# Kernel optimization log

Measured on AMD Instinct MI355X. Metric: run time of the kernel, lower is better.

Reference implementation:

```python
import jax, jax.numpy as jnp
import numpy as np

B, N_PER, E_PER = 100, 1000, 12000  # graphs, nodes/graph, edges/graph
N, E = B * N_PER, B * E_PER
K = int(np.ceil(0.8 * N_PER))  # TopKPooling ratio=0.8 -> 800 kept nodes/graph


def setup_inputs() -> dict:
    key = jax.random.key(0)
    ks = jax.random.split(key, 16)
    g = jnp.repeat(jnp.arange(B, dtype=jnp.int64), E_PER)
    src = g * N_PER + jax.random.randint(ks[0], (E,), 0, N_PER)
    dst = g * N_PER + jax.random.randint(ks[1], (E,), 0, N_PER)
    edge_index = jnp.stack([src, dst]).astype(jnp.int64)
    edge_attr = jax.random.uniform(ks[2], (E,), dtype=jnp.float32) + 0.1  # positive edge weights
    x = jax.random.normal(ks[3], (N, 3), dtype=jnp.float32)
    batch = jnp.repeat(jnp.arange(B, dtype=jnp.int64), N_PER)
    s = 0.1
    return {
        'x': x, 'edge_index': edge_index, 'edge_attr': edge_attr, 'batch': batch,
        'conv1_w': jax.random.normal(ks[4], (3, 64), dtype=jnp.float32) * s,
        'conv1_b': jnp.zeros((64,), dtype=jnp.float32),
        'conv2_w': jax.random.normal(ks[5], (64, 64), dtype=jnp.float32) * s,
        'conv2_b': jnp.zeros((64,), dtype=jnp.float32),
        'pool_w': jax.random.normal(ks[6], (64,), dtype=jnp.float32) * s,
        'lin1_w': jax.random.normal(ks[7], (64, 64), dtype=jnp.float32) * s,
        'lin1_b': jnp.zeros((64,), dtype=jnp.float32),
        'lin2_w': jax.random.normal(ks[8], (64, 32), dtype=jnp.float32) * s,
        'lin2_b': jnp.zeros((32,), dtype=jnp.float32),
        'lin3_w': jax.random.normal(ks[9], (32, 1), dtype=jnp.float32) * s,
        'lin3_b': jnp.zeros((1,), dtype=jnp.float32),
    }


def gcn_conv(x, row, col, ew, W, b):
    # PyG GCNConv with edge_weight and implicit self-loops (weight 1):
    # deg[i] = sum_{e: col=i} ew[e] + 1;  norm_e = d^{-1/2}[row]*ew*d^{-1/2}[col]
    h = x @ W  # [N, out]
    deg = jax.ops.segment_sum(ew, col, num_segments=N) + 1.0
    dinv = jax.lax.rsqrt(deg)
    msg = (dinv[row] * ew * dinv[col])[:, None] * h[row]  # [E, out]
    out = jax.ops.segment_sum(msg, col, num_segments=N)
    out = out + (dinv * dinv)[:, None] * h  # self-loop term
    return out + b


def reference(x, edge_index, edge_attr, batch, conv1_w, conv1_b, conv2_w, conv2_b,
              pool_w, lin1_w, lin1_b, lin2_w, lin2_b, lin3_w, lin3_b):
    row, col = edge_index[0], edge_index[1]
    h = jax.nn.relu(gcn_conv(x, row, col, edge_attr, conv1_w, conv1_b))
    x1 = h.reshape(B, N_PER, 64).mean(axis=1)  # global_mean_pool (equal-size graphs)
    h = jax.nn.relu(gcn_conv(h, row, col, edge_attr, conv2_w, conv2_b))
    # TopKPooling: score = tanh(x.w / ||w||), keep top-K per graph, gate by score
    score = jnp.tanh(h @ pool_w / jnp.linalg.norm(pool_w))  # [N]
    score_bn = score.reshape(B, N_PER)
    vals, idx = jax.lax.top_k(score_bn, K)  # [B, K]
    h_bn = h.reshape(B, N_PER, 64)
    h_sel = jnp.take_along_axis(h_bn, idx[..., None], axis=1) * vals[..., None]
    x2 = h_sel.mean(axis=1)  # global_mean_pool on pooled graph
    z = x1 + x2
    z = jax.nn.relu(z @ lin1_w + lin1_b)
    z = jax.nn.relu(z @ lin2_w + lin2_b)  # dropout is identity in eval mode
    out = jax.nn.sigmoid(z @ lin3_w + lin3_b)[:, 0]
    return out
```

## Files before the change

kernel.cpp:

```cpp
#include <hip/hip_runtime.h>

#define B_G   100
#define N_PER 1000
#define E_PER 12000
#define NTOT  (B_G * N_PER)
#define ETOT  (B_G * E_PER)
#define KSEL  800
#define EPT   12
#define NH    500
#define HCAP  8192

typedef __attribute__((ext_vector_type(8))) short short8;
typedef __attribute__((ext_vector_type(4))) float float4_;

__device__ __forceinline__ unsigned short f2bf(float f) {
    unsigned u = __float_as_uint(f);
    u += 0x7fffu + ((u >> 16) & 1u);
    return (unsigned short)(u >> 16);
}
__device__ __forceinline__ float upk(unsigned q) {
    return __uint_as_float(q & 0xFFFF0000u);
}
__device__ __forceinline__ float dec_raw(unsigned byte7f) {
    return __uint_as_float(byte7f << 20);
}
__device__ __forceinline__ unsigned enc_fp8(float z) {
    unsigned u = __float_as_uint(z * 0x1p-120f);
    u += 0x7FFFFu + ((u >> 20) & 1u);
    return u >> 20;
}

__global__ __launch_bounds__(1024) void k1_build(
    const int* __restrict__ ei, const float* __restrict__ ew,
    unsigned* __restrict__ csr_g, int* __restrict__ ends_g,
    float* __restrict__ dl_g) {
    __shared__ unsigned csr[E_PER];
    __shared__ int ends[1024];
    __shared__ int posc[1024];
    __shared__ int wpart[16];
    int b = blockIdx.x, tid = threadIdx.x;
    int wid = tid >> 6, lane = tid & 63;
    int gbase = b * N_PER, ebase = b * E_PER;

    int esrc[EPT], edst[EPT]; float eww[EPT];
    int ne = (tid < (E_PER - (EPT - 1) * 1024)) ? EPT : EPT - 1;
#pragma unroll
    for (int i = 0; i < EPT; i++) {
        if (i < ne) {
            int e = tid + i * 1024;
            esrc[i] = ei[ebase + e] - gbase;
            edst[i] = ei[ETOT + ebase + e] - gbase;
            eww[i]  = ew[ebase + e];
        }
    }
    ends[tid] = 0;
    __syncthreads();
#pragma unroll
    for (int i = 0; i < EPT; i++)
        if (i < ne) atomicAdd(&ends[edst[i]], 1);
    __syncthreads();
    int v = ends[tid], sc = v;
#pragma unroll
    for (int m = 1; m < 64; m <<= 1) {
        int t = __shfl_up(sc, m);
        if (lane >= m) sc += t;
    }
    if (lane == 63) wpart[wid] = sc;
    __syncthreads();
    if (tid < 16) {
        int s2 = wpart[tid];
#pragma unroll
        for (int m = 1; m < 16; m <<= 1) {
            int t = __shfl_up(s2, m);
            if (tid >= m) s2 += t;
        }
        wpart[tid] = s2;
    }
    __syncthreads();
    int incl = sc + (wid > 0 ? wpart[wid - 1] : 0);
    ends[tid] = incl;
    posc[tid] = incl - v;
    __syncthreads();
#pragma unroll
    for (int i = 0; i < EPT; i++)
        if (i < ne) {
            int p = atomicAdd(&posc[edst[i]], 1);
            csr[p] = ((unsigned)f2bf(eww[i]) << 16) | (unsigned)esrc[i];
        }
    __syncthreads();
    if (tid < N_PER) {
        int s = tid ? ends[tid - 1] : 0, e = ends[tid];
        float s0 = 0.f, s1 = 0.f;
        int k = s;
        for (; k + 2 <= e; k += 2) { s0 += upk(csr[k]); s1 += upk(csr[k + 1]); }
        if (k < e) s0 += upk(csr[k]);
        dl_g[gbase + tid] = rsqrtf(s0 + s1 + 1.0f);
        ends_g[gbase + tid] = e;
    }
    for (int i = tid; i < E_PER; i += 1024)
        csr_g[(size_t)ebase + i] = csr[i];
}

__global__ __launch_bounds__(1024) void k2_conv1(
    const float* __restrict__ x,
    const float* __restrict__ w1, const float* __restrict__ b1,
    const unsigned* __restrict__ csr_g, const int* __restrict__ ends_g,
    const float* __restrict__ dl_g,
    unsigned char* __restrict__ zg, float* __restrict__ x1g) {
    __shared__ float xl[3000];
    __shared__ unsigned csr[E_PER];
    __shared__ int ends[1024];
    __shared__ float dl[1024];
    __shared__ float aggv[3000];
    __shared__ float sred[1024];
    int b = blockIdx.x, tid = threadIdx.x;
    int wid = tid >> 6, lane = tid & 63;
    int gbase = b * N_PER, ebase = b * E_PER;

    for (int i = tid; i < N_PER * 3; i += 1024) xl[i] = x[(size_t)gbase * 3 + i];
    for (int i = tid; i < E_PER; i += 1024) csr[i] = csr_g[(size_t)ebase + i];
    if (tid < N_PER) {
        ends[tid] = ends_g[gbase + tid];
        dl[tid] = dl_g[gbase + tid];
    }
    __syncthreads();
    if (tid < N_PER) {
        float d = dl[tid];
        xl[tid * 3 + 0] *= d; xl[tid * 3 + 1] *= d; xl[tid * 3 + 2] *= d;
    }
    __syncthreads();
    if (tid < N_PER) {
        int s = tid ? ends[tid - 1] : 0, e = ends[tid];
        float a0 = xl[tid * 3 + 0], a1 = xl[tid * 3 + 1], a2 = xl[tid * 3 + 2];
        for (int k = s; k < e; k++) {
            unsigned q = csr[k];
            int i0 = (int)(q & 0xFFFFu) * 3;
            float wv = upk(q);
            a0 += wv * xl[i0]; a1 += wv * xl[i0 + 1]; a2 += wv * xl[i0 + 2];
        }
        float d = dl[tid];
        aggv[tid * 3 + 0] = d * a0;
        aggv[tid * 3 + 1] = d * a1;
        aggv[tid * 3 + 2] = d * a2;
    }
    __syncthreads();
    {
        float w0 = w1[lane], w1v = w1[64 + lane], w2v = w1[128 + lane], bf = b1[lane];
        float px = 0.f;
        int chunk = (lane & 31) >> 3;
        int word  = ((lane >= 32) ? 2 : 0) + ((lane & 7) >> 2);
        unsigned char* zrow = zg + (size_t)b * 64000;
        for (int node = wid; node < N_PER; node += 16) {
            float a0 = aggv[node * 3], a1 = aggv[node * 3 + 1], a2 = aggv[node * 3 + 2];
            float hv = fmaxf(a0 * w0 + a1 * w1v + a2 * w2v + bf, 0.f);
            px += hv;
            unsigned byte = enc_fp8(dl[node] * hv);
            unsigned t1 = __shfl_xor(byte, 1);
            unsigned v16 = (lane & 1) ? (t1 | (byte << 8)) : (byte | (t1 << 8));
            unsigned t2 = __shfl_xor(v16, 2);
            unsigned v32 = (lane & 2) ? (t2 | (v16 << 16)) : (v16 | (t2 << 16));
            if ((lane & 3) == 0) {
                int cs = chunk ^ ((node >> 1) & 3);
                *(unsigned*)(zrow + node * 64 + cs * 16 + word * 4) = v32;
            }
        }
        sred[wid * 64 + lane] = px;
        __syncthreads();
        if (tid < 64) {
            float t = 0.f;
            for (int r = 0; r < 16; r++) t += sred[r * 64 + tid];
            x1g[b * 64 + tid] = t * (1.0f / N_PER);
        }
    }
}

__global__ __launch_bounds__(1024) void k3_conv2(
    const unsigned char* __restrict__ zg, const unsigned* __restrict__ csr_g,
    const int* __restrict__ ends_g, const float* __restrict__ dl_g,
    const float* __restrict__ w2, const float* __restrict__ b2,
    const float* __restrict__ pw,
    unsigned char* __restrict__ h2g, float* __restrict__ score_g) {
    __shared__ __align__(16) unsigned char zs[64000];
    __shared__ unsigned csr[HCAP];
    __shared__ int ends[NH + 12];
    __shared__ float dl[NH + 12];
    __shared__ unsigned short w2s[64 * 64];
    int blk = blockIdx.x;
    int g = blk >> 1, h = blk & 1;
    int tid = threadIdx.x, wid = tid >> 6, lane = tid & 63;
    int kgrp = lane >> 4, nloc = lane & 15;
    int gbase = g * N_PER, nbase = h * NH;

    for (int i = tid; i < 64000 / 4; i += 1024)
        ((unsigned*)zs)[i] = ((const unsigned*)(zg + (size_t)g * 64000))[i];
    int base = h ? ends_g[gbase + NH - 1] : 0;
    int etot = ends_g[gbase + nbase + NH - 1];
    int nE = etot - base;
    if (tid < NH) {
        ends[tid] = ends_g[gbase + nbase + tid] - base;
        dl[tid] = dl_g[gbase + nbase + tid];
    }
    for (int i = tid; i < nE; i += 1024)
        csr[i] = csr_g[(size_t)g * E_PER + base + i];
    {
        int n = tid >> 4;
        for (int k = (tid & 15) * 4, ke = k + 4; k < ke; k++)
            w2s[n * 64 + k] = f2bf(w2[k * 64 + n]);
    }
    float b2c[4], pwc[4];
#pragma unroll
    for (int c = 0; c < 4; ++c) {
        b2c[c] = b2[c * 16 + nloc];
        pwc[c] = pw[c * 16 + nloc];
    }
    float invn;
    {
        float p = pw[lane], pn = p * p;
#pragma unroll
        for (int m = 32; m; m >>= 1) pn += __shfl_xor(pn, m);
        invn = rsqrtf(pn);
    }
    __syncthreads();
#pragma unroll 1
    for (int ti = 0; ti < 2; ti++) {
        int t = wid + ti * 16;
        int li = t * 16 + nloc;
        bool valid = li < NH;
        float acc[16];
        int s = 0, cn = 0;
        if (valid) {
            int gn = nbase + li;
            uint4 rv = *(const uint4*)(zs + gn * 64 + ((kgrp ^ ((gn >> 1) & 3)) << 4));
#pragma unroll
            for (int j = 0; j < 4; j++) {
                acc[j]      = dec_raw((rv.x >> (8 * j)) & 0x7Fu);
                acc[4 + j]  = dec_raw((rv.y >> (8 * j)) & 0x7Fu);
                acc[8 + j]  = dec_raw((rv.z >> (8 * j)) & 0x7Fu);
                acc[12 + j] = dec_raw((rv.w >> (8 * j)) & 0x7Fu);
            }
            s = li ? ends[li - 1] : 0;
            cn = ends[li] - s;
        } else {
#pragma unroll
            for (int j = 0; j < 16; j++) acc[j] = 0.f;
        }
        int mx = cn;
#pragma unroll
        for (int m = 1; m < 16; m <<= 1) mx = max(mx, __shfl_xor(mx, m));
        for (int k = 0; k < mx; k++) {
            if (k < cn) {
                unsigned q = csr[s + k];
                int src = (int)(q & 0xFFFFu);
                float wv = upk(q);
                uint4 rv = *(const uint4*)(zs + src * 64 + ((kgrp ^ ((src >> 1) & 3)) << 4));
#pragma unroll
                for (int j = 0; j < 4; j++) {
                    acc[j]      += wv * dec_raw((rv.x >> (8 * j)) & 0x7Fu);
                    acc[4 + j]  += wv * dec_raw((rv.y >> (8 * j)) & 0x7Fu);
                    acc[8 + j]  += wv * dec_raw((rv.z >> (8 * j)) & 0x7Fu);
                    acc[12 + j] += wv * dec_raw((rv.w >> (8 * j)) & 0x7Fu);
                }
            }
        }
        float scale = (valid ? dl[li] : 0.f) * 0x1p120f;
        short8 Af0, Af1;
#pragma unroll
        for (int j = 0; j < 8; j++) {
            Af0[j] = (short)f2bf(scale * acc[j]);
            Af1[j] = (short)f2bf(scale * acc[8 + j]);
        }
        float4_ accv[4];
#pragma unroll
        for (int c = 0; c < 4; ++c) {
            const short8* bp = (const short8*)(w2s + (c * 16 + nloc) * 64 + kgrp * 8);
            accv[c] = __builtin_amdgcn_mfma_f32_16x16x32_bf16(Af0, bp[0], (float4_){0.f,0.f,0.f,0.f}, 0, 0, 0);
            accv[c] = __builtin_amdgcn_mfma_f32_16x16x32_bf16(Af1, bp[4], accv[c], 0, 0, 0);
        }
#pragma unroll
        for (int r2 = 0; r2 < 4; ++r2) {
            int li2 = t * 16 + kgrp * 4 + r2;
            bool valid2 = li2 < NH;
            float sp = 0.f;
            unsigned pack = 0;
#pragma unroll
            for (int c = 0; c < 4; ++c) {
                float hv = fmaxf(accv[c][r2] + b2c[c], 0.f);
                sp += hv * pwc[c];
                pack |= enc_fp8(hv) << (8 * c);
            }
            if (valid2)
                *(unsigned*)(h2g + (size_t)(gbase + nbase + li2) * 64 + nloc * 4) = pack;
#pragma unroll
            for (int m = 1; m < 16; m <<= 1) sp += __shfl_xor(sp, m);
            if (valid2 && nloc == 0)
                score_g[gbase + nbase + li2] = tanhf(sp * invn);
        }
    }
}

__global__ __launch_bounds__(1024) void k4_topk(
    const float* __restrict__ score_g, const unsigned char* __restrict__ h2g,
    const float* __restrict__ x1g,
    const float* __restrict__ l1w, const float* __restrict__ l1b,
    const float* __restrict__ l2w, const float* __restrict__ l2b,
    const float* __restrict__ l3w, const float* __restrict__ l3b,
    float* __restrict__ out) {
    __shared__ unsigned long long keys[1024];
    __shared__ float red[1024];
    __shared__ float zbuf[64], a1buf[64], a2buf[32];
    int b = blockIdx.x, tid = threadIdx.x;
    if (tid < N_PER) {
        float scv = score_g[b * N_PER + tid];
        unsigned bits = __float_as_uint(scv);
        unsigned u = (bits & 0x80000000u) ? ~bits : (bits | 0x80000000u);
        keys[tid] = ((unsigned long long)u << 32) | (unsigned)(1023 - tid);
    } else {
        keys[tid] = 0ull;
    }
    __syncthreads();
    {
        unsigned long long key = keys[tid];
        for (int k = 2; k <= 1024; k <<= 1) {
            for (int j = k >> 1; j > 0; j >>= 1) {
                bool desc = (tid & k) == 0;
                unsigned long long p;
                if (j >= 64) {
                    keys[tid] = key;
                    __syncthreads();
                    p = keys[tid ^ j];
                    __syncthreads();
                } else {
                    p = __shfl_xor(key, j);
                }
                bool low = (tid & j) == 0;
                bool sw = low ? (desc ? (key < p) : (key > p))
                              : (desc ? (p < key) : (p > key));
                if (sw) key = p;
            }
        }
        keys[tid] = key;
    }
    __syncthreads();
    {
        int f = tid & 63, w16 = tid >> 6;
        int boff = ((f & 15) << 2) + (f >> 4);
        float acc2 = 0.f;
        for (int r = w16; r < KSEL; r += 16) {
            unsigned long long key = keys[r];
            int idx = 1023 - (int)(key & 0xFFFFFFFFu);
            unsigned u = (unsigned)(key >> 32);
            unsigned bits = (u & 0x80000000u) ? (u & 0x7FFFFFFFu) : ~u;
            float valS = __uint_as_float(bits) * 0x1p120f;
            acc2 += valS * dec_raw((unsigned)h2g[(size_t)(b * N_PER + idx) * 64 + boff] & 0x7Fu);
        }
        red[tid] = acc2;
    }
    __syncthreads();
    if (tid < 64) {
        float s2 = 0.f;
        for (int ww = 0; ww < 16; ww++) s2 += red[ww * 64 + tid];
        zbuf[tid] = x1g[b * 64 + tid] + s2 * (1.0f / KSEL);
    }
    __syncthreads();
    if (tid < 64) {
        float a = l1b[tid];
        for (int k = 0; k < 64; k++) a += zbuf[k] * l1w[k * 64 + tid];
        a1buf[tid] = fmaxf(a, 0.f);
    }
    __syncthreads();
    if (tid < 32) {
        float a = l2b[tid];
        for (int k = 0; k < 64; k++) a += a1buf[k] * l2w[k * 32 + tid];
        a2buf[tid] = fmaxf(a, 0.f);
    }
    __syncthreads();
    if (tid == 0) {
        float t = l3b[0];
        for (int k = 0; k < 32; k++) t += a2buf[k] * l3w[k];
        out[b] = 1.0f / (1.0f + expf(-t));
    }
}

extern "C" void kernel_launch(void* const* d_in, const int* in_sizes, int n_in,
                              void* d_out, int out_size, void* d_ws, size_t ws_size,
                              hipStream_t stream) {
    const float* x   = (const float*)d_in[0];
    const int*   ei  = (const int*)d_in[1];
    const float* ew  = (const float*)d_in[2];
    const float* c1w = (const float*)d_in[4];
    const float* c1b = (const float*)d_in[5];
    const float* c2w = (const float*)d_in[6];
    const float* c2b = (const float*)d_in[7];
    const float* pw  = (const float*)d_in[8];
    const float* l1w = (const float*)d_in[9];
    const float* l1b = (const float*)d_in[10];
    const float* l2w = (const float*)d_in[11];
    const float* l2b = (const float*)d_in[12];
    const float* l3w = (const float*)d_in[13];
    const float* l3b = (const float*)d_in[14];
    float* out = (float*)d_out;

    char* ws = (char*)d_ws;
    size_t o = 0;
    auto alloc = [&](size_t bytes) { size_t cur = o; o += (bytes + 511) & ~(size_t)511; return cur; };
    unsigned*      csr_g   = (unsigned*)(ws + alloc((size_t)ETOT * 4));
    unsigned char* zg      = (unsigned char*)(ws + alloc((size_t)NTOT * 64));
    unsigned char* h2g     = (unsigned char*)(ws + alloc((size_t)NTOT * 64));
    int*           ends_g  = (int*)(ws + alloc((size_t)NTOT * 4));
    float*         dl_g    = (float*)(ws + alloc((size_t)NTOT * 4));
    float*         score_g = (float*)(ws + alloc((size_t)NTOT * 4));
    float*         x1g     = (float*)(ws + alloc((size_t)B_G * 64 * 4));
    (void)ws_size; (void)in_sizes; (void)n_in; (void)out_size;

    k1_build<<<B_G, 1024, 0, stream>>>(ei, ew, csr_g, ends_g, dl_g);
    k2_conv1<<<B_G, 1024, 0, stream>>>(x, c1w, c1b, csr_g, ends_g, dl_g, zg, x1g);
    k3_conv2<<<B_G * 2, 1024, 0, stream>>>(zg, csr_g, ends_g, dl_g, c2w, c2b, pw, h2g, score_g);
    k4_topk <<<B_G, 1024, 0, stream>>>(score_g, h2g, x1g, l1w, l1b, l2w, l2b, l3w, l3b, out);
}
```

Baseline: 189.7 us.

## Split conv1 into four node-quarter blocks per graph with atomic mean pooling

The conv1 kernel now launches four 256-thread blocks per graph, each handling 250 destination nodes, instead of one 1024-thread block per graph. CSR edges are read directly from global memory rather than staged in shared memory, and the per-graph mean pool is accumulated with atomicAdd into x1g, which k1 now zeroes. The aim is better occupancy and more blocks across the CUs for a small kernel, at the cost of redundantly loading the node features four times per graph and relying on float atomics, which makes summation order nondeterministic.

```diff
diff --git a/kernel.cpp b/kernel.cpp
--- a/kernel.cpp
+++ b/kernel.cpp
@@ -33,7 +33,7 @@
 __global__ __launch_bounds__(1024) void k1_build(
     const int* __restrict__ ei, const float* __restrict__ ew,
     unsigned* __restrict__ csr_g, int* __restrict__ ends_g,
-    float* __restrict__ dl_g) {
+    float* __restrict__ dl_g, float* __restrict__ x1g) {
     __shared__ unsigned csr[E_PER];
     __shared__ int ends[1024];
     __shared__ int posc[1024];
@@ -54,6 +54,7 @@
         }
     }
     ends[tid] = 0;
+    if (tid < 64) x1g[b * 64 + tid] = 0.f;
     __syncthreads();
 #pragma unroll
     for (int i = 0; i < EPT; i++)
@@ -101,44 +102,38 @@
         csr_g[(size_t)ebase + i] = csr[i];
 }
 
-__global__ __launch_bounds__(1024) void k2_conv1(
+__global__ __launch_bounds__(256) void k2_conv1(
     const float* __restrict__ x,
     const float* __restrict__ w1, const float* __restrict__ b1,
     const unsigned* __restrict__ csr_g, const int* __restrict__ ends_g,
     const float* __restrict__ dl_g,
     unsigned char* __restrict__ zg, float* __restrict__ x1g) {
-    __shared__ float xl[3000];
-    __shared__ unsigned csr[E_PER];
-    __shared__ int ends[1024];
-    __shared__ float dl[1024];
-    __shared__ float aggv[3000];
-    __shared__ float sred[1024];
-    int b = blockIdx.x, tid = threadIdx.x;
-    int wid = tid >> 6, lane = tid & 63;
-    int gbase = b * N_PER, ebase = b * E_PER;
-
-    for (int i = tid; i < N_PER * 3; i += 1024) xl[i] = x[(size_t)gbase * 3 + i];
-    for (int i = tid; i < E_PER; i += 1024) csr[i] = csr_g[(size_t)ebase + i];
-    if (tid < N_PER) {
-        ends[tid] = ends_g[gbase + tid];
-        dl[tid] = dl_g[gbase + tid];
-    }
-    __syncthreads();
-    if (tid < N_PER) {
-        float d = dl[tid];
-        xl[tid * 3 + 0] *= d; xl[tid * 3 + 1] *= d; xl[tid * 3 + 2] *= d;
-    }
-    __syncthreads();
-    if (tid < N_PER) {
-        int s = tid ? ends[tid - 1] : 0, e = ends[tid];
-        float a0 = xl[tid * 3 + 0], a1 = xl[tid * 3 + 1], a2 = xl[tid * 3 + 2];
+    __shared__ float yl[3000];
+    __shared__ float dls[1000];
+    __shared__ float aggv[750];
+    __shared__ float sred[4][64];
+    int blk = blockIdx.x;
+    int g = blk >> 2, qt = blk & 3;
+    int tid = threadIdx.x, wid = tid >> 6, lane = tid & 63;
+    int gbase = g * N_PER, nbase = qt * 250;
+    size_t geb = (size_t)g * E_PER;
+
+    for (int i = tid; i < N_PER; i += 256) dls[i] = dl_g[gbase + i];
+    __syncthreads();
+    for (int i = tid; i < 3000; i += 256) yl[i] = x[(size_t)gbase * 3 + i] * dls[i / 3];
+    __syncthreads();
+    if (tid < 250) {
+        int n = nbase + tid;
+        int s = n ? ends_g[gbase + n - 1] : 0;
+        int e = ends_g[gbase + n];
+        float a0 = yl[n * 3 + 0], a1 = yl[n * 3 + 1], a2 = yl[n * 3 + 2];
         for (int k = s; k < e; k++) {
-            unsigned q = csr[k];
+            unsigned q = csr_g[geb + k];
             int i0 = (int)(q & 0xFFFFu) * 3;
             float wv = upk(q);
-            a0 += wv * xl[i0]; a1 += wv * xl[i0 + 1]; a2 += wv * xl[i0 + 2];
-        }
-        float d = dl[tid];
+            a0 += wv * yl[i0]; a1 += wv * yl[i0 + 1]; a2 += wv * yl[i0 + 2];
+        }
+        float d = dls[n];
         aggv[tid * 3 + 0] = d * a0;
         aggv[tid * 3 + 1] = d * a1;
         aggv[tid * 3 + 2] = d * a2;
@@ -149,12 +144,13 @@
         float px = 0.f;
         int chunk = (lane & 31) >> 3;
         int word  = ((lane >= 32) ? 2 : 0) + ((lane & 7) >> 2);
-        unsigned char* zrow = zg + (size_t)b * 64000;
-        for (int node = wid; node < N_PER; node += 16) {
-            float a0 = aggv[node * 3], a1 = aggv[node * 3 + 1], a2 = aggv[node * 3 + 2];
+        unsigned char* zrow = zg + (size_t)g * 64000;
+        for (int ln = wid; ln < 250; ln += 4) {
+            int node = nbase + ln;
+            float a0 = aggv[ln * 3], a1 = aggv[ln * 3 + 1], a2 = aggv[ln * 3 + 2];
             float hv = fmaxf(a0 * w0 + a1 * w1v + a2 * w2v + bf, 0.f);
             px += hv;
-            unsigned byte = enc_fp8(dl[node] * hv);
+            unsigned byte = enc_fp8(dls[node] * hv);
             unsigned t1 = __shfl_xor(byte, 1);
             unsigned v16 = (lane & 1) ? (t1 | (byte << 8)) : (byte | (t1 << 8));
             unsigned t2 = __shfl_xor(v16, 2);
@@ -164,12 +160,11 @@
                 *(unsigned*)(zrow + node * 64 + cs * 16 + word * 4) = v32;
             }
         }
-        sred[wid * 64 + lane] = px;
+        sred[wid][lane] = px;
         __syncthreads();
         if (tid < 64) {
-            float t = 0.f;
-            for (int r = 0; r < 16; r++) t += sred[r * 64 + tid];
-            x1g[b * 64 + tid] = t * (1.0f / N_PER);
+            float t = sred[0][tid] + sred[1][tid] + sred[2][tid] + sred[3][tid];
+            atomicAdd(&x1g[g * 64 + tid], t * (1.0f / N_PER));
         }
     }
 }
@@ -412,8 +407,8 @@
     float*         x1g     = (float*)(ws + alloc((size_t)B_G * 64 * 4));
     (void)ws_size; (void)in_sizes; (void)n_in; (void)out_size;
 
-    k1_build<<<B_G, 1024, 0, stream>>>(ei, ew, csr_g, ends_g, dl_g);
-    k2_conv1<<<B_G, 1024, 0, stream>>>(x, c1w, c1b, csr_g, ends_g, dl_g, zg, x1g);
+    k1_build<<<B_G, 1024, 0, stream>>>(ei, ew, csr_g, ends_g, dl_g, x1g);
+    k2_conv1<<<B_G * 4, 256, 0, stream>>>(x, c1w, c1b, csr_g, ends_g, dl_g, zg, x1g);
     k3_conv2<<<B_G * 2, 1024, 0, stream>>>(zg, csr_g, ends_g, dl_g, c2w, c2b, pw, h2g, score_g);
     k4_topk <<<B_G, 1024, 0, stream>>>(score_g, h2g, x1g, l1w, l1b, l2w, l2b, l3w, l3b, out);
 }
```

Result: no change. 186.3 us (-1.8%).

## Split CSR build per half-graph and switch conv1 output to per-graph uint8 scaling

Applied to the files above, without the earlier changes.

The CSR build kernel now runs two blocks per graph, each keeping only edges whose destination falls in its half, with a fixed-capacity per-half CSR layout in global memory. Conv1 reads CSR straight from global memory instead of staging it in shared memory, and it quantizes its output to unsigned 8-bit with a per-graph max scale instead of the custom exponent-based fp8 encoding. Conv2 decodes these bytes with integer-to-float conversion and applies the stored scale. This doubles build parallelism and cuts shared memory use in conv1, but every edge is now read twice in the build, conv1 needs an extra pass to find the max, and the quantization error changes.

```diff
diff --git a/kernel.cpp b/kernel.cpp
--- a/kernel.cpp
+++ b/kernel.cpp
@@ -8,7 +8,7 @@
 #define KSEL  800
 #define EPT   12
 #define NH    500
-#define HCAP  8192
+#define CAPH  8192
 
 typedef __attribute__((ext_vector_type(8))) short short8;
 typedef __attribute__((ext_vector_type(4))) float float4_;
@@ -34,13 +34,15 @@
     const int* __restrict__ ei, const float* __restrict__ ew,
     unsigned* __restrict__ csr_g, int* __restrict__ ends_g,
     float* __restrict__ dl_g) {
-    __shared__ unsigned csr[E_PER];
+    __shared__ unsigned csr[CAPH];
     __shared__ int ends[1024];
     __shared__ int posc[1024];
     __shared__ int wpart[16];
-    int b = blockIdx.x, tid = threadIdx.x;
-    int wid = tid >> 6, lane = tid & 63;
-    int gbase = b * N_PER, ebase = b * E_PER;
+    int blk = blockIdx.x;
+    int g = blk >> 1, h = blk & 1;
+    int tid = threadIdx.x, wid = tid >> 6, lane = tid & 63;
+    int gbase = g * N_PER, ebase = g * E_PER;
+    int nb0 = h * NH;
 
     int esrc[EPT], edst[EPT]; float eww[EPT];
     int ne = (tid < (E_PER - (EPT - 1) * 1024)) ? EPT : EPT - 1;
@@ -49,7 +51,7 @@
         if (i < ne) {
             int e = tid + i * 1024;
             esrc[i] = ei[ebase + e] - gbase;
-            edst[i] = ei[ETOT + ebase + e] - gbase;
+            edst[i] = ei[ETOT + ebase + e] - gbase - nb0;
             eww[i]  = ew[ebase + e];
         }
     }
@@ -57,7 +59,7 @@
     __syncthreads();
 #pragma unroll
     for (int i = 0; i < EPT; i++)
-        if (i < ne) atomicAdd(&ends[edst[i]], 1);
+        if (i < ne && (unsigned)edst[i] < NH) atomicAdd(&ends[edst[i]], 1);
     __syncthreads();
     int v = ends[tid], sc = v;
 #pragma unroll
@@ -83,22 +85,24 @@
     __syncthreads();
 #pragma unroll
     for (int i = 0; i < EPT; i++)
-        if (i < ne) {
+        if (i < ne && (unsigned)edst[i] < NH) {
             int p = atomicAdd(&posc[edst[i]], 1);
-            csr[p] = ((unsigned)f2bf(eww[i]) << 16) | (unsigned)esrc[i];
-        }
-    __syncthreads();
-    if (tid < N_PER) {
+            if (p < CAPH)
+                csr[p] = ((unsigned)f2bf(eww[i]) << 16) | (unsigned)esrc[i];
+        }
+    __syncthreads();
+    if (tid < NH) {
         int s = tid ? ends[tid - 1] : 0, e = ends[tid];
         float s0 = 0.f, s1 = 0.f;
         int k = s;
         for (; k + 2 <= e; k += 2) { s0 += upk(csr[k]); s1 += upk(csr[k + 1]); }
         if (k < e) s0 += upk(csr[k]);
-        dl_g[gbase + tid] = rsqrtf(s0 + s1 + 1.0f);
-        ends_g[gbase + tid] = e;
-    }
-    for (int i = tid; i < E_PER; i += 1024)
-        csr_g[(size_t)ebase + i] = csr[i];
+        dl_g[gbase + nb0 + tid] = rsqrtf(s0 + s1 + 1.0f);
+        ends_g[gbase + nb0 + tid] = e;
+    }
+    int nE = ends[NH - 1];
+    for (int i = tid; i < nE; i += 1024)
+        csr_g[(size_t)blk * CAPH + i] = csr[i];
 }
 
 __global__ __launch_bounds__(1024) void k2_conv1(
@@ -106,55 +110,81 @@
     const float* __restrict__ w1, const float* __restrict__ b1,
     const unsigned* __restrict__ csr_g, const int* __restrict__ ends_g,
     const float* __restrict__ dl_g,
-    unsigned char* __restrict__ zg, float* __restrict__ x1g) {
-    __shared__ float xl[3000];
-    __shared__ unsigned csr[E_PER];
-    __shared__ int ends[1024];
-    __shared__ float dl[1024];
+    unsigned char* __restrict__ zg, float* __restrict__ x1g,
+    float* __restrict__ zscale_g) {
+    __shared__ float yl[3000];
+    __shared__ float dls[1000];
     __shared__ float aggv[3000];
     __shared__ float sred[1024];
-    int b = blockIdx.x, tid = threadIdx.x;
+    __shared__ float zmaxs;
+    int g = blockIdx.x, tid = threadIdx.x;
     int wid = tid >> 6, lane = tid & 63;
-    int gbase = b * N_PER, ebase = b * E_PER;
-
-    for (int i = tid; i < N_PER * 3; i += 1024) xl[i] = x[(size_t)gbase * 3 + i];
-    for (int i = tid; i < E_PER; i += 1024) csr[i] = csr_g[(size_t)ebase + i];
-    if (tid < N_PER) {
-        ends[tid] = ends_g[gbase + tid];
-        dl[tid] = dl_g[gbase + tid];
-    }
-    __syncthreads();
-    if (tid < N_PER) {
-        float d = dl[tid];
-        xl[tid * 3 + 0] *= d; xl[tid * 3 + 1] *= d; xl[tid * 3 + 2] *= d;
-    }
-    __syncthreads();
-    if (tid < N_PER) {
-        int s = tid ? ends[tid - 1] : 0, e = ends[tid];
-        float a0 = xl[tid * 3 + 0], a1 = xl[tid * 3 + 1], a2 = xl[tid * 3 + 2];
+    int gbase = g * N_PER;
+
+    for (int i = tid; i < 1000; i += 1024) dls[i] = dl_g[gbase + i];
+    __syncthreads();
+    for (int i = tid; i < 3000; i += 1024) yl[i] = x[(size_t)gbase * 3 + i] * dls[i / 3];
+    __syncthreads();
+    if (tid < 1000) {
+        int h = tid >= NH;
+        int loc = tid - h * NH;
+        size_t rb = ((size_t)g * 2 + h) * CAPH;
+        int s = loc ? ends_g[gbase + tid - 1] : 0;
+        int e = ends_g[gbase + tid];
+        float a0 = yl[tid * 3 + 0], a1 = yl[tid * 3 + 1], a2 = yl[tid * 3 + 2];
         for (int k = s; k < e; k++) {
-            unsigned q = csr[k];
+            unsigned q = csr_g[rb + k];
             int i0 = (int)(q & 0xFFFFu) * 3;
             float wv = upk(q);
-            a0 += wv * xl[i0]; a1 += wv * xl[i0 + 1]; a2 += wv * xl[i0 + 2];
-        }
-        float d = dl[tid];
+            a0 += wv * yl[i0]; a1 += wv * yl[i0 + 1]; a2 += wv * yl[i0 + 2];
+        }
+        float d = dls[tid];
         aggv[tid * 3 + 0] = d * a0;
         aggv[tid * 3 + 1] = d * a1;
         aggv[tid * 3 + 2] = d * a2;
     }
     __syncthreads();
-    {
-        float w0 = w1[lane], w1v = w1[64 + lane], w2v = w1[128 + lane], bf = b1[lane];
-        float px = 0.f;
-        int chunk = (lane & 31) >> 3;
-        int word  = ((lane >= 32) ? 2 : 0) + ((lane & 7) >> 2);
-        unsigned char* zrow = zg + (size_t)b * 64000;
-        for (int node = wid; node < N_PER; node += 16) {
+    float w0 = w1[lane], w1v = w1[64 + lane], w2v = w1[128 + lane], bf = b1[lane];
+    {
+        float px = 0.f, zmx = 0.f;
+        for (int node = wid; node < 1000; node += 16) {
             float a0 = aggv[node * 3], a1 = aggv[node * 3 + 1], a2 = aggv[node * 3 + 2];
             float hv = fmaxf(a0 * w0 + a1 * w1v + a2 * w2v + bf, 0.f);
             px += hv;
-            unsigned byte = enc_fp8(dl[node] * hv);
+            zmx = fmaxf(zmx, dls[node] * hv);
+        }
+        sred[tid] = px;
+        __syncthreads();
+        if (tid < 64) {
+            float t = 0.f;
+            for (int r = 0; r < 16; r++) t += sred[r * 64 + tid];
+            x1g[g * 64 + tid] = t * (1.0f / N_PER);
+        }
+        __syncthreads();
+        sred[tid] = zmx;
+        __syncthreads();
+        if (tid < 64) {
+            float m = sred[tid];
+            for (int r = 1; r < 16; r++) m = fmaxf(m, sred[r * 64 + tid]);
+#pragma unroll
+            for (int off = 32; off; off >>= 1) m = fmaxf(m, __shfl_xor(m, off));
+            if (tid == 0) {
+                zmaxs = m;
+                zscale_g[g] = m * (1.0f / 255.0f);
+            }
+        }
+        __syncthreads();
+    }
+    {
+        float s255 = (zmaxs > 0.f) ? 255.0f / zmaxs : 0.f;
+        int chunk = (lane & 31) >> 3;
+        int word  = ((lane >= 32) ? 2 : 0) + ((lane & 7) >> 2);
+        unsigned char* zrow = zg + (size_t)g * 64000;
+        for (int node = wid; node < 1000; node += 16) {
+            float a0 = aggv[node * 3], a1 = aggv[node * 3 + 1], a2 = aggv[node * 3 + 2];
+            float hv = fmaxf(a0 * w0 + a1 * w1v + a2 * w2v + bf, 0.f);
+            float zq = dls[node] * hv * s255 + 0.5f;
+            unsigned byte = (unsigned)fminf(zq, 255.f);
             unsigned t1 = __shfl_xor(byte, 1);
             unsigned v16 = (lane & 1) ? (t1 | (byte << 8)) : (byte | (t1 << 8));
             unsigned t2 = __shfl_xor(v16, 2);
@@ -164,26 +194,20 @@
                 *(unsigned*)(zrow + node * 64 + cs * 16 + word * 4) = v32;
             }
         }
-        sred[wid * 64 + lane] = px;
-        __syncthreads();
-        if (tid < 64) {
-            float t = 0.f;
-            for (int r = 0; r < 16; r++) t += sred[r * 64 + tid];
-            x1g[b * 64 + tid] = t * (1.0f / N_PER);
-        }
     }
 }
 
 __global__ __launch_bounds__(1024) void k3_conv2(
     const unsigned char* __restrict__ zg, const unsigned* __restrict__ csr_g,
     const int* __restrict__ ends_g, const float* __restrict__ dl_g,
+    const float* __restrict__ zscale_g,
     const float* __restrict__ w2, const float* __restrict__ b2,
     const float* __restrict__ pw,
     unsigned char* __restrict__ h2g, float* __restrict__ score_g) {
     __shared__ __align__(16) unsigned char zs[64000];
-    __shared__ unsigned csr[HCAP];
-    __shared__ int ends[NH + 12];
-    __shared__ float dl[NH + 12];
+    __shared__ unsigned csr[CAPH];
+    __shared__ int ends[NH];
+    __shared__ float dl[NH];
     __shared__ unsigned short w2s[64 * 64];
     int blk = blockIdx.x;
     int g = blk >> 1, h = blk & 1;
@@ -193,15 +217,13 @@
 
     for (int i = tid; i < 64000 / 4; i += 1024)
         ((unsigned*)zs)[i] = ((const unsigned*)(zg + (size_t)g * 64000))[i];
-    int base = h ? ends_g[gbase + NH - 1] : 0;
-    int etot = ends_g[gbase + nbase + NH - 1];
-    int nE = etot - base;
+    int nE = ends_g[gbase + nbase + NH - 1];
     if (tid < NH) {
-        ends[tid] = ends_g[gbase + nbase + tid] - base;
+        ends[tid] = ends_g[gbase + nbase + tid];
         dl[tid] = dl_g[gbase + nbase + tid];
     }
     for (int i = tid; i < nE; i += 1024)
-        csr[i] = csr_g[(size_t)g * E_PER + base + i];
+        csr[i] = csr_g[((size_t)g * 2 + h) * CAPH + i];
     {
         int n = tid >> 4;
         for (int k = (tid & 15) * 4, ke = k + 4; k < ke; k++)
@@ -220,6 +242,7 @@
         for (int m = 32; m; m >>= 1) pn += __shfl_xor(pn, m);
         invn = rsqrtf(pn);
     }
+    float zsc = zscale_g[g];
     __syncthreads();
 #pragma unroll 1
     for (int ti = 0; ti < 2; ti++) {
@@ -233,10 +256,10 @@
             uint4 rv = *(const uint4*)(zs + gn * 64 + ((kgrp ^ ((gn >> 1) & 3)) << 4));
 #pragma unroll
             for (int j = 0; j < 4; j++) {
-                acc[j]      = dec_raw((rv.x >> (8 * j)) & 0x7Fu);
-                acc[4 + j]  = dec_raw((rv.y >> (8 * j)) & 0x7Fu);
-                acc[8 + j]  = dec_raw((rv.z >> (8 * j)) & 0x7Fu);
-                acc[12 + j] = dec_raw((rv.w >> (8 * j)) & 0x7Fu);
+                acc[j]      = (float)((rv.x >> (8 * j)) & 0xFFu);
+                acc[4 + j]  = (float)((rv.y >> (8 * j)) & 0xFFu);
+                acc[8 + j]  = (float)((rv.z >> (8 * j)) & 0xFFu);
+                acc[12 + j] = (float)((rv.w >> (8 * j)) & 0xFFu);
             }
             s = li ? ends[li - 1] : 0;
             cn = ends[li] - s;
@@ -255,14 +278,14 @@
                 uint4 rv = *(const uint4*)(zs + src * 64 + ((kgrp ^ ((src >> 1) & 3)) << 4));
 #pragma unroll
                 for (int j = 0; j < 4; j++) {
-                    acc[j]      += wv * dec_raw((rv.x >> (8 * j)) & 0x7Fu);
-                    acc[4 + j]  += wv * dec_raw((rv.y >> (8 * j)) & 0x7Fu);
-                    acc[8 + j]  += wv * dec_raw((rv.z >> (8 * j)) & 0x7Fu);
-                    acc[12 + j] += wv * dec_raw((rv.w >> (8 * j)) & 0x7Fu);
+                    acc[j]      += wv * (float)((rv.x >> (8 * j)) & 0xFFu);
+                    acc[4 + j]  += wv * (float)((rv.y >> (8 * j)) & 0xFFu);
+                    acc[8 + j]  += wv * (float)((rv.z >> (8 * j)) & 0xFFu);
+                    acc[12 + j] += wv * (float)((rv.w >> (8 * j)) & 0xFFu);
                 }
             }
         }
-        float scale = (valid ? dl[li] : 0.f) * 0x1p120f;
+        float scale = (valid ? dl[li] : 0.f) * zsc;
         short8 Af0, Af1;
 #pragma unroll
         for (int j = 0; j < 8; j++) {
@@ -403,17 +426,18 @@
     char* ws = (char*)d_ws;
     size_t o = 0;
     auto alloc = [&](size_t bytes) { size_t cur = o; o += (bytes + 511) & ~(size_t)511; return cur; };
-    unsigned*      csr_g   = (unsigned*)(ws + alloc((size_t)ETOT * 4));
-    unsigned char* zg      = (unsigned char*)(ws + alloc((size_t)NTOT * 64));
-    unsigned char* h2g     = (unsigned char*)(ws + alloc((size_t)NTOT * 64));
-    int*           ends_g  = (int*)(ws + alloc((size_t)NTOT * 4));
-    float*         dl_g    = (float*)(ws + alloc((size_t)NTOT * 4));
-    float*         score_g = (float*)(ws + alloc((size_t)NTOT * 4));
-    float*         x1g     = (float*)(ws + alloc((size_t)B_G * 64 * 4));
+    unsigned*      csr_g    = (unsigned*)(ws + alloc((size_t)B_G * 2 * CAPH * 4));
+    unsigned char* zg       = (unsigned char*)(ws + alloc((size_t)NTOT * 64));
+    unsigned char* h2g      = (unsigned char*)(ws + alloc((size_t)NTOT * 64));
+    int*           ends_g   = (int*)(ws + alloc((size_t)NTOT * 4));
+    float*         dl_g     = (float*)(ws + alloc((size_t)NTOT * 4));
+    float*         score_g  = (float*)(ws + alloc((size_t)NTOT * 4));
+    float*         x1g      = (float*)(ws + alloc((size_t)B_G * 64 * 4));
+    float*         zscale_g = (float*)(ws + alloc((size_t)B_G * 4));
     (void)ws_size; (void)in_sizes; (void)n_in; (void)out_size;
 
-    k1_build<<<B_G, 1024, 0, stream>>>(ei, ew, csr_g, ends_g, dl_g);
-    k2_conv1<<<B_G, 1024, 0, stream>>>(x, c1w, c1b, csr_g, ends_g, dl_g, zg, x1g);
-    k3_conv2<<<B_G * 2, 1024, 0, stream>>>(zg, csr_g, ends_g, dl_g, c2w, c2b, pw, h2g, score_g);
+    k1_build<<<B_G * 2, 1024, 0, stream>>>(ei, ew, csr_g, ends_g, dl_g);
+    k2_conv1<<<B_G, 1024, 0, stream>>>(x, c1w, c1b, csr_g, ends_g, dl_g, zg, x1g, zscale_g);
+    k3_conv2<<<B_G * 2, 1024, 0, stream>>>(zg, csr_g, ends_g, dl_g, zscale_g, c2w, c2b, pw, h2g, score_g);
     k4_topk <<<B_G, 1024, 0, stream>>>(score_g, h2g, x1g, l1w, l1b, l2w, l2b, l3w, l3b, out);
 }
```

New measurement: 185.4 us. 2.3% less time.
